# Performance work log

Measured on AMD Instinct MI355X. Metric: run time of the kernel, lower is better.

Reference implementation:

```python
import jax, jax.numpy as jnp
import numpy as np

PUSH_MARGIN = 1.0
NUM_LABELS = 65  # label ids 0..64; 0 = background (skipped)
EPS = 1e-12


def _safe_norm(d, axis):
    # L2 norm with grad-safe sqrt at 0 (matches ||.||_2 value everywhere relevant)
    sq = jnp.sum(d * d, axis=axis)
    return jnp.sqrt(jnp.maximum(sq, EPS))


def setup_inputs() -> dict:
    key = jax.random.key(0)
    k1, k2, k3 = jax.random.split(key, 3)
    B, N, C, H, W = 16, 16384, 128, 512, 512
    abs_embedding = jax.random.normal(k1, (B, N, C), dtype=jnp.float32)
    coordinates = jax.random.randint(k2, (B, N, 2), 0, H, dtype=jnp.int32)
    y = jax.random.randint(k3, (B, H, W), 0, NUM_LABELS, dtype=jnp.int32)
    return {"abs_embedding": abs_embedding, "coordinates": coordinates, "y": y}


def reference(abs_embedding, coordinates, y):
    def per_image(emb, coords, yb):
        # emb: [N,C], coords: [N,2], yb: [H,W]
        labels = yb[coords[:, 0], coords[:, 1]]                       # [N]
        ones = jnp.ones(labels.shape, emb.dtype)
        counts = jax.ops.segment_sum(ones, labels, num_segments=NUM_LABELS)   # [L]
        sums = jax.ops.segment_sum(emb, labels, num_segments=NUM_LABELS)      # [L,C]
        centroids = sums / jnp.maximum(counts, 1.0)[:, None]                   # [L,C]
        # pull: per-instance mean distance of samples to their centroid, summed over fg instances
        d = _safe_norm(emb - centroids[labels], axis=-1)              # [N]
        dist_sum = jax.ops.segment_sum(d, labels, num_segments=NUM_LABELS)
        fg_counts = counts[1:]
        present = fg_counts > 0
        pull = jnp.sum(jnp.where(present, dist_sum[1:] / jnp.maximum(fg_counts, 1.0), 0.0))
        # push: mean over strict-upper-tri pairs of relu(margin - ||c_i - c_j||)
        c = centroids[1:]                                             # [K,C]
        dm = _safe_norm(c[:, None, :] - c[None, :, :], axis=-1)        # [K,K]
        push_vals = jax.nn.relu(PUSH_MARGIN - dm)
        K = c.shape[0]
        tri = jnp.triu(jnp.ones((K, K), bool), k=1)
        pair_mask = tri & present[:, None] & present[None, :]
        npairs = jnp.maximum(jnp.sum(pair_mask.astype(emb.dtype)), 1.0)
        push = jnp.sum(jnp.where(pair_mask, push_vals, 0.0)) / npairs
        return pull + push

    per_b = jax.vmap(per_image)(abs_embedding, coordinates, y)        # [B]
    return jnp.sum(per_b)
```

## Files before the change

kernel.cpp:

```cpp
#include <hip/hip_runtime.h>

#define B_ 16
#define N_ 16384
#define C_ 128
#define H_ 512
#define W_ 512
#define L_ 65
#define FG 64

#define OFF_SUMS 0
#define OFF_CNT  (B_*L_*C_)
#define OFF_DIST (OFF_CNT + B_*L_)
#define OFF_LAB  (OFF_DIST + B_*L_)
#define OFF_BCNT (OFF_LAB + B_*N_)
#define OFF_PART (OFF_BCNT + 1024*L_)

#define APB 512
#define DPB 256
#define PREP_BLOCKS (B_*N_/256)

__global__ __launch_bounds__(256) void k_prep(const int2* __restrict__ coords,
                                              const int* __restrict__ y,
                                              float* __restrict__ ws,
                                              float* __restrict__ out) {
    __shared__ int s_cnt[L_];
    const int gid = blockIdx.x * 256 + threadIdx.x;
    if (threadIdx.x < L_) s_cnt[threadIdx.x] = 0;
    if (gid < B_ * L_) ws[OFF_DIST + gid] = 0.f;
    if (gid == 0) out[0] = 0.f;
    __syncthreads();
    const int b = gid >> 14;
    int2 rc = coords[gid];
    int lab = y[(b << 18) + (rc.x << 9) + rc.y];
    ((int*)(ws + OFF_LAB))[gid] = lab;
    atomicAdd(&s_cnt[lab], 1);
    __syncthreads();
    if (threadIdx.x < L_)
        ((int*)(ws + OFF_BCNT))[blockIdx.x * L_ + threadIdx.x] = s_cnt[threadIdx.x];
}

__global__ __launch_bounds__(256) void k_accum(const float* __restrict__ emb,
                                               float* __restrict__ ws) {
    __shared__ float4 s_sum4[2 * L_ * 32];
    __shared__ int s_lab[APB];
    const int b = blockIdx.x >> 5;
    const int base = (blockIdx.x & 31) * APB;
    const int wave = threadIdx.x >> 6;
    const int lane = threadIdx.x & 63;
    const int half = lane >> 5, j = lane & 31;

    const float4 zero4 = {0.f, 0.f, 0.f, 0.f};
    for (int i = threadIdx.x; i < 2 * L_ * 32; i += 256) s_sum4[i] = zero4;
    const int* labg = (const int*)(ws + OFF_LAB) + b * N_ + base;
    for (int i = threadIdx.x; i < APB; i += 256) s_lab[i] = labg[i];
    __syncthreads();

    const float4* embp = (const float4*)(emb + (size_t)b * N_ * C_
                                         + (size_t)(base + wave * (APB / 4)) * C_) + j;
    const int* labp = s_lab + wave * (APB / 4);
    float4* copy = s_sum4 + half * (L_ * 32) + j;

#define LOADB(e, lb, s) do {                                   \
        _Pragma("unroll")                                      \
        for (int u = 0; u < 8; ++u) {                          \
            int p = 2 * ((s) * 8 + u) + half;                  \
            e[u]  = embp[(size_t)p * 32];   \
            lb[u] = labp[p];                \
        } } while (0)

#define RMWB(e, lb) do {                                       \
        _Pragma("unroll")                                      \
        for (int u = 0; u < 8; ++u) {                          \
            float4 v = copy[lb[u] * 32];                       \
            v.x += e[u].x; v.y += e[u].y;                      \
            v.z += e[u].z; v.w += e[u].w;                      \
            copy[lb[u] * 32] = v;                              \
        } } while (0)

    float4 eA[8], eB[8]; int lbA[8], lbB[8];
    LOADB(eA, lbA, 0);
    LOADB(eB, lbB, 1);
    RMWB(eA, lbA);
    LOADB(eA, lbA, 2);
    RMWB(eB, lbB);
    LOADB(eB, lbB, 3);
    RMWB(eA, lbA);
    LOADB(eA, lbA, 4);
    RMWB(eB, lbB);
    LOADB(eB, lbB, 5);
    RMWB(eA, lbA);
    LOADB(eA, lbA, 6);
    RMWB(eB, lbB);
    LOADB(eB, lbB, 7);
    RMWB(eA, lbA);
    RMWB(eB, lbB);
#undef LOADB
#undef RMWB

    __syncthreads();
    float4* gp4 = (float4*)(ws + OFF_PART) + (size_t)blockIdx.x * (L_ * 32);
    for (int i = threadIdx.x; i < L_ * 32; i += 256) {
        float4 a = s_sum4[i], c = s_sum4[L_ * 32 + i];
        a.x += c.x; a.y += c.y; a.z += c.z; a.w += c.w;
        gp4[i] = a;
    }
}

__global__ __launch_bounds__(256) void k_cent(float* __restrict__ ws) {
    __shared__ float s_inv[L_];
    const int b = blockIdx.x >> 3, c = blockIdx.x & 7;
    const int t = threadIdx.x;
    if (t < L_) {
        const int* bc = (const int*)(ws + OFF_BCNT);
        int cnt = 0;
        #pragma unroll 8
        for (int k = 0; k < PREP_BLOCKS / B_; ++k)
            cnt += bc[(b * (PREP_BLOCKS / B_) + k) * L_ + t];
        if (c == 0) ((int*)(ws + OFF_CNT))[b * L_ + t] = cnt;
        s_inv[t] = 1.f / fmaxf((float)cnt, 1.f);
    }
    __syncthreads();
    const float4* part = (const float4*)(ws + OFF_PART) + (size_t)b * 32 * (L_ * 32);
    float4* gs = (float4*)(ws + OFF_SUMS) + (size_t)b * (L_ * 32);
    for (int i4 = c * 260 + t; i4 < (c + 1) * 260 && i4 < L_ * 32; i4 += 256) {
        float4 s = {0.f, 0.f, 0.f, 0.f};
        #pragma unroll 8
        for (int s0 = 0; s0 < 32; ++s0) {
            float4 p = part[(size_t)s0 * (L_ * 32) + i4];
            s.x += p.x; s.y += p.y; s.z += p.z; s.w += p.w;
        }
        float inv = s_inv[(i4 * 4) >> 7];
        s.x *= inv; s.y *= inv; s.z *= inv; s.w *= inv;
        gs[i4] = s;
    }
}

__global__ __launch_bounds__(256) void k_dist(const float* __restrict__ emb,
                                              float* __restrict__ ws) {
    __shared__ __align__(16) float4 s_cent4[L_ * 33];
    __shared__ float s_dist[L_];
    const int b = blockIdx.x >> 6;
    const int base = (blockIdx.x & 63) * DPB;

    const float* gcent = ws + OFF_SUMS + b * L_ * C_;
    for (int i = threadIdx.x; i < L_ * 32; i += 256) {
        int l = i >> 5, q = i & 31;
        s_cent4[l * 33 + q] = ((const float4*)gcent)[l * 32 + q];
    }
    if (threadIdx.x < L_) s_dist[threadIdx.x] = 0.f;
    __syncthreads();

    const int p = base + threadIdx.x;
    const int lb = ((const int*)(ws + OFF_LAB))[b * N_ + p];
    const float4* ep = (const float4*)(emb + (size_t)b * N_ * C_) + (size_t)p * 32;
    const float4* cp = s_cent4 + lb * 33;
    float acc = 0.f;
    #pragma unroll 8
    for (int q = 0; q < 32; ++q) {
        float4 e = ep[q], c = cp[q];
        float dx = e.x - c.x, dy = e.y - c.y;
        float dz = e.z - c.z, dw = e.w - c.w;
        acc += dx * dx + dy * dy + dz * dz + dw * dw;
    }
    unsafeAtomicAdd(&s_dist[lb], sqrtf(fmaxf(acc, 1e-12f)));
    __syncthreads();
    if (threadIdx.x < L_) {
        float d = s_dist[threadIdx.x];
        if (d != 0.f) unsafeAtomicAdd(ws + OFF_DIST + b * L_ + threadIdx.x, d);
    }
}

#define CSTRIDE 132

__global__ __launch_bounds__(256) void k_final(float* __restrict__ ws, float* __restrict__ out) {
    __shared__ __align__(16) float s_cc[FG * CSTRIDE];
    __shared__ float s_present[FG];
    __shared__ float s_red[3];
    const int b = blockIdx.x;
    const int t = threadIdx.x;

    const float* gcent = ws + OFF_SUMS + b * L_ * C_;
    for (int i = t; i < FG * C_; i += 256) {
        int l = i >> 7, ch = i & 127;
        s_cc[l * CSTRIDE + ch] = gcent[(l + 1) * C_ + ch];
    }
    if (t < 3) s_red[t] = 0.f;
    if (t < FG) {
        int cnt = ((const int*)(ws + OFF_CNT))[b * L_ + 1 + t];
        s_present[t] = (cnt > 0) ? 1.f : 0.f;
        float pl = (cnt > 0) ? ws[OFF_DIST + b * L_ + 1 + t] / (float)cnt : 0.f;
        #pragma unroll
        for (int off = 32; off; off >>= 1) pl += __shfl_xor(pl, off);
        if (t == 0) s_red[0] = pl;
    }
    __syncthreads();

    const int wave = t >> 6, lane = t & 63;
    const int ti = lane >> 3, tj = lane & 7;
    float psum = 0.f, pnp = 0.f;
    for (int tt = wave; tt < 36; tt += 4) {
        int a = 0, c = tt;
        while (c >= 8 - a) { c -= 8 - a; ++a; }
        c += a;
        int i = a * 8 + ti, jx = c * 8 + tj;
        float acc = 0.f;
        #pragma unroll
        for (int ch = 0; ch < C_; ch += 4) {
            float4 xi = *(const float4*)&s_cc[i * CSTRIDE + ch];
            float4 xj = *(const float4*)&s_cc[jx * CSTRIDE + ch];
            float dx = xi.x - xj.x, dy = xi.y - xj.y;
            float dz = xi.z - xj.z, dw = xi.w - xj.w;
            acc += dx * dx + dy * dy + dz * dz + dw * dw;
        }
        float dm = sqrtf(fmaxf(acc, 1e-12f));
        float pv = fmaxf(1.f - dm, 0.f);
        bool valid = (i < jx) && (s_present[i] > 0.f) && (s_present[jx] > 0.f);
        if (valid) { psum += pv; pnp += 1.f; }
    }
    #pragma unroll
    for (int off = 32; off; off >>= 1) {
        psum += __shfl_xor(psum, off);
        pnp  += __shfl_xor(pnp,  off);
    }
    if (lane == 0) { unsafeAtomicAdd(&s_red[1], psum); unsafeAtomicAdd(&s_red[2], pnp); }
    __syncthreads();
    if (t == 0) {
        float loss = s_red[0] + s_red[1] / fmaxf(s_red[2], 1.f);
        unsafeAtomicAdd(out, loss);
    }
}

extern "C" void kernel_launch(void* const* d_in, const int* in_sizes, int n_in,
                              void* d_out, int out_size, void* d_ws, size_t ws_size,
                              hipStream_t stream) {
    const float* emb   = (const float*)d_in[0];
    const int2* coords = (const int2*)d_in[1];
    const int*  y      = (const int*)d_in[2];
    float* out = (float*)d_out;
    float* ws  = (float*)d_ws;

    k_prep<<<PREP_BLOCKS, 256, 0, stream>>>(coords, y, ws, out);
    k_accum<<<B_ * (N_ / APB), 256, 0, stream>>>(emb, ws);
    k_cent<<<B_ * 8, 256, 0, stream>>>(ws);
    k_dist<<<B_ * (N_ / DPB), 256, 0, stream>>>(emb, ws);
    k_final<<<B_, 256, 0, stream>>>(ws, out);
}
```

Measured before the change: 253.0 us.

## Fuse label gather and counting into accumulation kernel; widen distance kernel blocks

```diff
diff --git a/kernel.cpp b/kernel.cpp
--- a/kernel.cpp
+++ b/kernel.cpp
@@ -16,44 +16,38 @@
 #define OFF_PART (OFF_BCNT + 1024*L_)
 
 #define APB 512
-#define DPB 256
-#define PREP_BLOCKS (B_*N_/256)
-
-__global__ __launch_bounds__(256) void k_prep(const int2* __restrict__ coords,
-                                              const int* __restrict__ y,
-                                              float* __restrict__ ws,
-                                              float* __restrict__ out) {
-    __shared__ int s_cnt[L_];
-    const int gid = blockIdx.x * 256 + threadIdx.x;
-    if (threadIdx.x < L_) s_cnt[threadIdx.x] = 0;
-    if (gid < B_ * L_) ws[OFF_DIST + gid] = 0.f;
-    if (gid == 0) out[0] = 0.f;
-    __syncthreads();
-    const int b = gid >> 14;
-    int2 rc = coords[gid];
-    int lab = y[(b << 18) + (rc.x << 9) + rc.y];
-    ((int*)(ws + OFF_LAB))[gid] = lab;
-    atomicAdd(&s_cnt[lab], 1);
-    __syncthreads();
-    if (threadIdx.x < L_)
-        ((int*)(ws + OFF_BCNT))[blockIdx.x * L_ + threadIdx.x] = s_cnt[threadIdx.x];
-}
+#define DPB 1024
 
 __global__ __launch_bounds__(256) void k_accum(const float* __restrict__ emb,
+                                               const int2* __restrict__ coords,
+                                               const int* __restrict__ y,
                                                float* __restrict__ ws) {
     __shared__ float4 s_sum4[2 * L_ * 32];
     __shared__ int s_lab[APB];
+    __shared__ int s_cnt[L_];
     const int b = blockIdx.x >> 5;
     const int base = (blockIdx.x & 31) * APB;
-    const int wave = threadIdx.x >> 6;
-    const int lane = threadIdx.x & 63;
+    const int t = threadIdx.x;
+    const int wave = t >> 6;
+    const int lane = t & 63;
     const int half = lane >> 5, j = lane & 31;
 
+    const int g0 = b * N_ + base + t, g1 = g0 + 256;
+    int2 r0 = coords[g0], r1 = coords[g1];
+    if (t < L_) s_cnt[t] = 0;
     const float4 zero4 = {0.f, 0.f, 0.f, 0.f};
-    for (int i = threadIdx.x; i < 2 * L_ * 32; i += 256) s_sum4[i] = zero4;
-    const int* labg = (const int*)(ws + OFF_LAB) + b * N_ + base;
-    for (int i = threadIdx.x; i < APB; i += 256) s_lab[i] = labg[i];
-    __syncthreads();
+    for (int i = t; i < 2 * L_ * 32; i += 256) s_sum4[i] = zero4;
+    int l0 = y[(b << 18) + (r0.x << 9) + r0.y];
+    int l1 = y[(b << 18) + (r1.x << 9) + r1.y];
+    __syncthreads();
+    s_lab[t] = l0; s_lab[t + 256] = l1;
+    ((int*)(ws + OFF_LAB))[g0] = l0;
+    ((int*)(ws + OFF_LAB))[g1] = l1;
+    atomicAdd(&s_cnt[l0], 1);
+    atomicAdd(&s_cnt[l1], 1);
+    __syncthreads();
+    if (t < L_)
+        ((int*)(ws + OFF_BCNT))[blockIdx.x * L_ + t] = s_cnt[t];
 
     const float4* embp = (const float4*)(emb + (size_t)b * N_ * C_
                                          + (size_t)(base + wave * (APB / 4)) * C_) + j;
@@ -99,23 +93,26 @@
 
     __syncthreads();
     float4* gp4 = (float4*)(ws + OFF_PART) + (size_t)blockIdx.x * (L_ * 32);
-    for (int i = threadIdx.x; i < L_ * 32; i += 256) {
+    for (int i = t; i < L_ * 32; i += 256) {
         float4 a = s_sum4[i], c = s_sum4[L_ * 32 + i];
         a.x += c.x; a.y += c.y; a.z += c.z; a.w += c.w;
         gp4[i] = a;
     }
 }
 
-__global__ __launch_bounds__(256) void k_cent(float* __restrict__ ws) {
+__global__ __launch_bounds__(256) void k_cent(float* __restrict__ ws,
+                                              float* __restrict__ out) {
     __shared__ float s_inv[L_];
     const int b = blockIdx.x >> 3, c = blockIdx.x & 7;
     const int t = threadIdx.x;
+    if (c == 0 && t < L_) ws[OFF_DIST + b * L_ + t] = 0.f;
+    if (blockIdx.x == 0 && t == 0) out[0] = 0.f;
     if (t < L_) {
         const int* bc = (const int*)(ws + OFF_BCNT);
         int cnt = 0;
         #pragma unroll 8
-        for (int k = 0; k < PREP_BLOCKS / B_; ++k)
-            cnt += bc[(b * (PREP_BLOCKS / B_) + k) * L_ + t];
+        for (int k = 0; k < 32; ++k)
+            cnt += bc[(b * 32 + k) * L_ + t];
         if (c == 0) ((int*)(ws + OFF_CNT))[b * L_ + t] = cnt;
         s_inv[t] = 1.f / fmaxf((float)cnt, 1.f);
     }
@@ -135,38 +132,47 @@
     }
 }
 
-__global__ __launch_bounds__(256) void k_dist(const float* __restrict__ emb,
+__global__ __launch_bounds__(512) void k_dist(const float* __restrict__ emb,
                                               float* __restrict__ ws) {
     __shared__ __align__(16) float4 s_cent4[L_ * 33];
     __shared__ float s_dist[L_];
-    const int b = blockIdx.x >> 6;
-    const int base = (blockIdx.x & 63) * DPB;
+    const int b = blockIdx.x >> 4;
+    const int base = (blockIdx.x & 15) * DPB;
+    const int t = threadIdx.x;
 
     const float* gcent = ws + OFF_SUMS + b * L_ * C_;
-    for (int i = threadIdx.x; i < L_ * 32; i += 256) {
+    for (int i = t; i < L_ * 32; i += 512) {
         int l = i >> 5, q = i & 31;
         s_cent4[l * 33 + q] = ((const float4*)gcent)[l * 32 + q];
     }
-    if (threadIdx.x < L_) s_dist[threadIdx.x] = 0.f;
-    __syncthreads();
-
-    const int p = base + threadIdx.x;
-    const int lb = ((const int*)(ws + OFF_LAB))[b * N_ + p];
-    const float4* ep = (const float4*)(emb + (size_t)b * N_ * C_) + (size_t)p * 32;
-    const float4* cp = s_cent4 + lb * 33;
-    float acc = 0.f;
-    #pragma unroll 8
+    if (t < L_) s_dist[t] = 0.f;
+    __syncthreads();
+
+    const int p0 = base + t, p1 = p0 + 512;
+    const int* labp = (const int*)(ws + OFF_LAB) + b * N_;
+    const int lb0 = labp[p0], lb1 = labp[p1];
+    const float4* e0 = (const float4*)(emb + (size_t)b * N_ * C_) + (size_t)p0 * 32;
+    const float4* e1 = e0 + (size_t)512 * 32;
+    const float4* c0 = s_cent4 + lb0 * 33;
+    const float4* c1 = s_cent4 + lb1 * 33;
+    float a0 = 0.f, a1 = 0.f;
+    #pragma unroll 4
     for (int q = 0; q < 32; ++q) {
-        float4 e = ep[q], c = cp[q];
-        float dx = e.x - c.x, dy = e.y - c.y;
-        float dz = e.z - c.z, dw = e.w - c.w;
-        acc += dx * dx + dy * dy + dz * dz + dw * dw;
-    }
-    unsafeAtomicAdd(&s_dist[lb], sqrtf(fmaxf(acc, 1e-12f)));
-    __syncthreads();
-    if (threadIdx.x < L_) {
-        float d = s_dist[threadIdx.x];
-        if (d != 0.f) unsafeAtomicAdd(ws + OFF_DIST + b * L_ + threadIdx.x, d);
+        float4 x0 = e0[q], y0 = c0[q];
+        float4 x1 = e1[q], y1 = c1[q];
+        float dx0 = x0.x - y0.x, dy0 = x0.y - y0.y;
+        float dz0 = x0.z - y0.z, dw0 = x0.w - y0.w;
+        float dx1 = x1.x - y1.x, dy1 = x1.y - y1.y;
+        float dz1 = x1.z - y1.z, dw1 = x1.w - y1.w;
+        a0 += dx0 * dx0 + dy0 * dy0 + dz0 * dz0 + dw0 * dw0;
+        a1 += dx1 * dx1 + dy1 * dy1 + dz1 * dz1 + dw1 * dw1;
+    }
+    unsafeAtomicAdd(&s_dist[lb0], sqrtf(fmaxf(a0, 1e-12f)));
+    unsafeAtomicAdd(&s_dist[lb1], sqrtf(fmaxf(a1, 1e-12f)));
+    __syncthreads();
+    if (t < L_) {
+        float d = s_dist[t];
+        if (d != 0.f) unsafeAtomicAdd(ws + OFF_DIST + b * L_ + t, d);
     }
 }
 
@@ -239,9 +245,8 @@
     float* out = (float*)d_out;
     float* ws  = (float*)d_ws;
 
-    k_prep<<<PREP_BLOCKS, 256, 0, stream>>>(coords, y, ws, out);
-    k_accum<<<B_ * (N_ / APB), 256, 0, stream>>>(emb, ws);
-    k_cent<<<B_ * 8, 256, 0, stream>>>(ws);
-    k_dist<<<B_ * (N_ / DPB), 256, 0, stream>>>(emb, ws);
+    k_accum<<<B_ * (N_ / APB), 256, 0, stream>>>(emb, coords, y, ws);
+    k_cent<<<B_ * 8, 256, 0, stream>>>(ws, out);
+    k_dist<<<B_ * (N_ / DPB), 512, 0, stream>>>(emb, ws);
     k_final<<<B_, 256, 0, stream>>>(ws, out);
 }
```

Measured after the change: 266.9 us. 5.5% more time.
